# Kernel optimization log

Hardware: AMD Instinct MI355X
Metric: run time of the kernel (lower is better)

Reference implementation:

```python
import jax, jax.numpy as jnp
import numpy as np
import math

B, C, N = 8, 512, 2048

def setup_inputs() -> dict:
    key = jax.random.key(0)
    ks = jax.random.split(key, 7)
    s = 0.02
    return {
        "x": jax.random.normal(ks[0], (B, C, N), dtype=jnp.float32),
        "Wq": jax.random.normal(ks[1], (C // 2, C), dtype=jnp.float32) * s,
        "bq": jax.random.normal(ks[2], (C // 2,), dtype=jnp.float32) * s,
        "Wk": jax.random.normal(ks[3], (C // 2, C), dtype=jnp.float32) * s,
        "bk": jax.random.normal(ks[4], (C // 2,), dtype=jnp.float32) * s,
        "Wv": jax.random.normal(ks[5], (C, C), dtype=jnp.float32) * s,
        "bv": jax.random.normal(ks[6], (C,), dtype=jnp.float32) * s,
    }

def reference(x, Wq, bq, Wk, bk, Wv, bv):
    # pointwise conv1d == channel matmul: (O,C) x (B,C,N) -> (B,O,N)
    Q = jnp.einsum('oc,bcn->bon', Wq, x) + bq[None, :, None]  # (B, C/2, N)
    K = jnp.einsum('oc,bcn->bon', Wk, x) + bk[None, :, None]  # (B, C/2, N)
    V = jnp.einsum('oc,bcn->bon', Wv, x) + bv[None, :, None]  # (B, C, N)
    scale = 1.0 / math.sqrt(K.shape[1])
    A = jnp.einsum('bcn,bcm->bnm', Q, K) * scale              # (B, N, N)
    A = jax.nn.softmax(A, axis=-1)
    out = jnp.einsum('bcm,bnm->bcn', V, A)                    # V @ A^T
    return x + out
```

## Files before the change

### kernel.cpp

```cpp
#include <hip/hip_runtime.h>

#define B_ 8
#define C_ 512
#define N_ 2048
#define O_ 256

typedef unsigned short u16;
typedef unsigned char u8;
typedef unsigned int uint;
typedef __bf16 bf16x8 __attribute__((ext_vector_type(8)));
typedef float f32x4 __attribute__((ext_vector_type(4)));
typedef int i32x8 __attribute__((ext_vector_type(8)));

#define AS1 __attribute__((address_space(1)))
#define AS3 __attribute__((address_space(3)))

__device__ __forceinline__ u16 f2bf(float f) {
  union { float f; unsigned u; } v; v.f = f;
  return (u16)((v.u + 0x7fffu + ((v.u >> 16) & 1u)) >> 16);
}

__device__ __forceinline__ uint pk4_e4m3(float a, float b, float c, float d) {
  int r = __builtin_amdgcn_cvt_pk_fp8_f32(a, b, 0, false);
  r = __builtin_amdgcn_cvt_pk_fp8_f32(c, d, r, true);
  return (uint)r;
}

__device__ __forceinline__ void mfma_mainloop(
    const u16* __restrict__ Ag, int lda,
    const u16* __restrict__ Bg, int ldb, int K,
    u16 (&As)[128][64], u16 (&Bs)[128][64], f32x4 (&acc)[4][4])
{
  const int t = threadIdx.x;
  const int lane = t & 63;
  const int w = t >> 6;
  const int wm = (w >> 1) * 64, wn = (w & 1) * 64;
  const int lrow = lane & 15, quad = lane >> 4;
  const int r8 = lane >> 3;
  const int kgsrc = (lane & 7) ^ r8;
  const int swz = lrow & 7;

  for (int k0 = 0; k0 < K; k0 += 64) {
#pragma unroll
    for (int i = 0; i < 4; i++) {
      int row = w * 32 + i * 8;
      __builtin_amdgcn_global_load_lds(
          (const AS1 uint*)(Ag + (size_t)(row + r8) * lda + k0 + kgsrc * 8),
          (AS3 uint*)(&As[row][0]), 16, 0, 0);
      __builtin_amdgcn_global_load_lds(
          (const AS1 uint*)(Bg + (size_t)(row + r8) * ldb + k0 + kgsrc * 8),
          (AS3 uint*)(&Bs[row][0]), 16, 0, 0);
    }
    __syncthreads();
#pragma unroll
    for (int kk = 0; kk < 2; kk++) {
      const int pg = (kk * 4 + quad) ^ swz;
      bf16x8 af[4], bfr[4];
#pragma unroll
      for (int i = 0; i < 4; i++)
        af[i] = *(const bf16x8*)(&As[wm + i * 16 + lrow][pg * 8]);
#pragma unroll
      for (int j = 0; j < 4; j++)
        bfr[j] = *(const bf16x8*)(&Bs[wn + j * 16 + lrow][pg * 8]);
#pragma unroll
      for (int i = 0; i < 4; i++)
#pragma unroll
        for (int j = 0; j < 4; j++)
          acc[i][j] = __builtin_amdgcn_mfma_f32_16x16x32_bf16(af[i], bfr[j], acc[i][j], 0, 0, 0);
    }
    __syncthreads();
  }
}

union MxFrag { i32x8 v; uint4 q[2]; };

__device__ __forceinline__ void mx_mainloop(
    const u8* __restrict__ Ag, int lda,
    const u8* __restrict__ Bg, int ldb, int K,
    u8 (&As)[128][128], u8 (&Bs)[128][128], f32x4 (&acc)[4][4])
{
  const int t = threadIdx.x;
  const int lane = t & 63;
  const int w = t >> 6;
  const int wm = (w >> 1) * 64, wn = (w & 1) * 64;
  const int lrow = lane & 15, quad = lane >> 4;
  const int swz = lrow & 7;
  const int r8 = lane >> 3;
  const int gsrc = (lane & 7) ^ r8;

  for (int k0 = 0; k0 < K; k0 += 128) {
#pragma unroll
    for (int i = 0; i < 4; i++) {
      int row = i * 32 + w * 8;
      __builtin_amdgcn_global_load_lds(
          (const AS1 uint*)(Ag + (size_t)(row + r8) * lda + k0 + gsrc * 16),
          (AS3 uint*)(&As[row][0]), 16, 0, 0);
      __builtin_amdgcn_global_load_lds(
          (const AS1 uint*)(Bg + (size_t)(row + r8) * ldb + k0 + gsrc * 16),
          (AS3 uint*)(&Bs[row][0]), 16, 0, 0);
    }
    __syncthreads();
    const int g0 = (quad * 2) ^ swz, g1 = (quad * 2 + 1) ^ swz;
    MxFrag af[4], bfr[4];
#pragma unroll
    for (int i = 0; i < 4; i++) {
      const u8* rp = &As[wm + i * 16 + lrow][0];
      af[i].q[0] = *(const uint4*)(rp + g0 * 16);
      af[i].q[1] = *(const uint4*)(rp + g1 * 16);
    }
#pragma unroll
    for (int j = 0; j < 4; j++) {
      const u8* rp = &Bs[wn + j * 16 + lrow][0];
      bfr[j].q[0] = *(const uint4*)(rp + g0 * 16);
      bfr[j].q[1] = *(const uint4*)(rp + g1 * 16);
    }
#pragma unroll
    for (int i = 0; i < 4; i++)
#pragma unroll
      for (int j = 0; j < 4; j++)
        acc[i][j] = __builtin_amdgcn_mfma_scale_f32_16x16x128_f8f6f4(
            af[i].v, bfr[j].v, acc[i][j],
            0, 0,
            0, 0x7f7f7f7f,
            0, 0x7f7f7f7f);
    __syncthreads();
  }
}

__global__ __launch_bounds__(256) void convert_w_kernel(
    const float* __restrict__ Wq, const float* __restrict__ Wk,
    const float* __restrict__ Wv,
    u16* __restrict__ Wqb, u16* __restrict__ Wkb, u16* __restrict__ Wvb,
    float* __restrict__ rowsum)
{
  int i = blockIdx.x * 256 + threadIdx.x;
  if (i < O_ * C_) { Wqb[i] = f2bf(Wq[i]); Wkb[i] = f2bf(Wk[i]); }
  Wvb[i] = f2bf(Wv[i]);
  if (i < B_ * N_) rowsum[i] = 0.f;
}

__global__ __launch_bounds__(256) void transpose_kernel(
    const float* __restrict__ x, u16* __restrict__ xT)
{
  __shared__ u16 tile[64][72];
  int b = blockIdx.z;
  int n0 = blockIdx.x * 64, c0 = blockIdx.y * 64;
  int t = threadIdx.x;
  const float* src = x + (size_t)b * C_ * N_ + (size_t)c0 * N_ + n0;
  int r = t >> 4;
  int f4 = (t & 15) * 4;
#pragma unroll
  for (int i = 0; i < 4; i++) {
    int c = r + 16 * i;
    float4 v = *(const float4*)(src + (size_t)c * N_ + f4);
    tile[f4 + 0][c] = f2bf(v.x);
    tile[f4 + 1][c] = f2bf(v.y);
    tile[f4 + 2][c] = f2bf(v.z);
    tile[f4 + 3][c] = f2bf(v.w);
  }
  __syncthreads();
  u16* dst = xT + (size_t)b * N_ * C_ + (size_t)n0 * C_ + c0;
  int nr = t >> 3;
  int cc = (t & 7) * 8;
#pragma unroll
  for (int i = 0; i < 2; i++) {
    int n = nr + 32 * i;
    *(uint4*)(dst + (size_t)n * C_ + cc) = *(const uint4*)(&tile[n][cc]);
  }
}

__global__ __launch_bounds__(256) void proj_all_kernel(
    const u16* __restrict__ xT,
    const u16* __restrict__ Wqb, const float* __restrict__ bq,
    const u16* __restrict__ Wkb, const float* __restrict__ bk,
    const u16* __restrict__ Wvb, const float* __restrict__ bv,
    u8* __restrict__ Qt8, u8* __restrict__ Kt8, u8* __restrict__ V8)
{
  __shared__ u16 As[128][64], Bs[128][64];
  const int n0 = blockIdx.x * 128;
  const int b = blockIdx.y;
  const int sub = blockIdx.z;
  const u16* xTb = xT + (size_t)b * N_ * C_ + (size_t)n0 * C_;

  const f32x4 zero = {0.f, 0.f, 0.f, 0.f};
  f32x4 acc[4][4];
#pragma unroll
  for (int i = 0; i < 4; i++)
#pragma unroll
    for (int j = 0; j < 4; j++) acc[i][j] = zero;

  const int lane = threadIdx.x & 63;
  const int w = threadIdx.x >> 6;
  const int wm = (w >> 1) * 64, wn = (w & 1) * 64;
  const int quad = lane >> 4, lcol = lane & 15;

  if (sub < 4) {
    const int isK = sub >> 1;
    const int o0 = (sub & 1) * 128;
    const u16* Wg = (isK ? Wkb : Wqb) + (size_t)o0 * C_;
    const float* bias = isK ? bk : bq;
    u8* outp = (isK ? Kt8 : Qt8) + (size_t)b * N_ * O_;

    mfma_mainloop(Wg, C_, xTb, C_, C_, As, Bs, acc);

#pragma unroll
    for (int i = 0; i < 4; i++) {
      int obase = o0 + wm + i * 16 + quad * 4;
      float4 bb = *(const float4*)(bias + obase);
#pragma unroll
      for (int j = 0; j < 4; j++) {
        int n = n0 + wn + j * 16 + lcol;
        uint d = pk4_e4m3(acc[i][j][0] + bb.x, acc[i][j][1] + bb.y,
                          acc[i][j][2] + bb.z, acc[i][j][3] + bb.w);
        *(uint*)(outp + (size_t)n * O_ + obase) = d;
      }
    }
  } else {
    const int c0 = (sub - 4) * 128;
    const u16* Wg = Wvb + (size_t)c0 * C_;
    u8* outp = V8 + (size_t)b * C_ * N_;

    mfma_mainloop(xTb, C_, Wg, C_, C_, As, Bs, acc);

#pragma unroll
    for (int j = 0; j < 4; j++) {
      int c = c0 + wn + j * 16 + lcol;
      float bb = bv[c];
#pragma unroll
      for (int i = 0; i < 4; i++) {
        int nbase = n0 + wm + i * 16 + quad * 4;
        uint d = pk4_e4m3(acc[i][j][0] + bb, acc[i][j][1] + bb,
                          acc[i][j][2] + bb, acc[i][j][3] + bb);
        *(uint*)(outp + (size_t)c * N_ + nbase) = d;
      }
    }
  }
}

__global__ __launch_bounds__(256) void attn_s_kernel(
    const u8* __restrict__ Qt8, const u8* __restrict__ Kt8,
    u8* __restrict__ P, float* __restrict__ rowsum)
{
  __shared__ __align__(16) u8 As[128][128], Bs[128][128];
  int b = blockIdx.z;
  int m0 = blockIdx.x * 128, n0 = blockIdx.y * 128;
  const u8* Ag = Kt8 + (size_t)b * N_ * O_ + (size_t)m0 * O_;
  const u8* Bg = Qt8 + (size_t)b * N_ * O_ + (size_t)n0 * O_;

  const f32x4 zero = {0.f, 0.f, 0.f, 0.f};
  f32x4 acc[4][4];
#pragma unroll
  for (int i = 0; i < 4; i++)
#pragma unroll
    for (int j = 0; j < 4; j++) acc[i][j] = zero;

  mx_mainloop(Ag, O_, Bg, O_, O_, As, Bs, acc);

  u8* Pp = P + (size_t)b * N_ * N_;
  float* rs = rowsum + (size_t)b * N_;
  const int lane = threadIdx.x & 63;
  const int w = threadIdx.x >> 6;
  const int wm = (w >> 1) * 64, wn = (w & 1) * 64;
  const int quad = lane >> 4, lcol = lane & 15;

  float partial[4];
#pragma unroll
  for (int j = 0; j < 4; j++) partial[j] = 0.f;

#pragma unroll
  for (int j = 0; j < 4; j++) {
    int n = n0 + wn + j * 16 + lcol;
#pragma unroll
    for (int i = 0; i < 4; i++) {
      int mbase = m0 + wm + i * 16 + quad * 4;
      float p0 = __expf(acc[i][j][0] * 0.0625f);
      float p1 = __expf(acc[i][j][1] * 0.0625f);
      float p2 = __expf(acc[i][j][2] * 0.0625f);
      float p3 = __expf(acc[i][j][3] * 0.0625f);
      *(uint*)(Pp + (size_t)n * N_ + mbase) = pk4_e4m3(p0, p1, p2, p3);
      partial[j] += p0 + p1 + p2 + p3;
    }
  }
#pragma unroll
  for (int msk = 16; msk < 64; msk <<= 1)
#pragma unroll
    for (int j = 0; j < 4; j++)
      partial[j] += __shfl_xor(partial[j], msk);
  if (quad == 0) {
#pragma unroll
    for (int j = 0; j < 4; j++)
      atomicAdd(&rs[n0 + wn + j * 16 + lcol], partial[j]);
  }
}

__global__ __launch_bounds__(256) void attn_o_kernel(
    const u8* __restrict__ V, const u8* __restrict__ P,
    const float* __restrict__ rowsum, const float* __restrict__ x,
    float* __restrict__ out)
{
  __shared__ __align__(16) u8 As[128][128], Bs[128][128];
  int b = blockIdx.z;
  int c0 = blockIdx.y * 128, n0 = blockIdx.x * 128;
  const u8* Ag = V + (size_t)b * C_ * N_ + (size_t)c0 * N_;
  const u8* Bg = P + (size_t)b * N_ * N_ + (size_t)n0 * N_;

  const f32x4 zero = {0.f, 0.f, 0.f, 0.f};
  f32x4 acc[4][4];
#pragma unroll
  for (int i = 0; i < 4; i++)
#pragma unroll
    for (int j = 0; j < 4; j++) acc[i][j] = zero;

  mx_mainloop(Ag, N_, Bg, N_, N_, As, Bs, acc);

  const int lane = threadIdx.x & 63;
  const int w = threadIdx.x >> 6;
  const int wm = (w >> 1) * 64, wn = (w & 1) * 64;
  const int quad = lane >> 4, lrow = lane & 15;

  const float* xb = x + (size_t)b * C_ * N_;
  float* ob = out + (size_t)b * C_ * N_;
  float invl[4];
#pragma unroll
  for (int j = 0; j < 4; j++)
    invl[j] = 1.f / rowsum[b * N_ + n0 + wn + j * 16 + lrow];

#pragma unroll
  for (int i = 0; i < 4; i++)
#pragma unroll
    for (int rr = 0; rr < 4; rr++) {
      int c = c0 + wm + i * 16 + quad * 4 + rr;
#pragma unroll
      for (int j = 0; j < 4; j++) {
        int n = n0 + wn + j * 16 + lrow;
        size_t idx = (size_t)c * N_ + n;
        ob[idx] = xb[idx] + acc[i][j][rr] * invl[j];
      }
    }
}

extern "C" void kernel_launch(void* const* d_in, const int* in_sizes, int n_in,
                              void* d_out, int out_size, void* d_ws, size_t ws_size,
                              hipStream_t stream)
{
  (void)in_sizes; (void)n_in; (void)out_size; (void)ws_size;
  const float* x  = (const float*)d_in[0];
  const float* Wq = (const float*)d_in[1];
  const float* bq = (const float*)d_in[2];
  const float* Wk = (const float*)d_in[3];
  const float* bk = (const float*)d_in[4];
  const float* Wv = (const float*)d_in[5];
  const float* bv = (const float*)d_in[6];
  float* out = (float*)d_out;

  char* ws = (char*)d_ws;
  size_t off = 0;
  auto carve = [&](size_t bytes) -> char* {
    char* p = ws + off;
    off += (bytes + 255) & ~(size_t)255;
    return p;
  };
  u16* xT   = (u16*)carve((size_t)B_ * N_ * C_ * 2);
  u16* Wqb  = (u16*)carve((size_t)O_ * C_ * 2);
  u16* Wkb  = (u16*)carve((size_t)O_ * C_ * 2);
  u16* Wvb  = (u16*)carve((size_t)C_ * C_ * 2);
  u8*  Qt8  = (u8*) carve((size_t)B_ * N_ * O_);
  u8*  Kt8  = (u8*) carve((size_t)B_ * N_ * O_);
  u8*  Vb   = (u8*) carve((size_t)B_ * C_ * N_);
  u8*  P    = (u8*) carve((size_t)B_ * N_ * N_);
  float* rowsum = (float*)carve((size_t)B_ * N_ * 4);

  convert_w_kernel<<<dim3((C_ * C_) / 256), 256, 0, stream>>>(
      Wq, Wk, Wv, Wqb, Wkb, Wvb, rowsum);
  transpose_kernel<<<dim3(N_ / 64, C_ / 64, B_), 256, 0, stream>>>(x, xT);
  proj_all_kernel<<<dim3(N_ / 128, B_, 8), 256, 0, stream>>>(
      xT, Wqb, bq, Wkb, bk, Wvb, bv, Qt8, Kt8, Vb);
  attn_s_kernel<<<dim3(N_ / 128, N_ / 128, B_), 256, 0, stream>>>(Qt8, Kt8, P, rowsum);
  attn_o_kernel<<<dim3(N_ / 128, C_ / 128, B_), 256, 0, stream>>>(Vb, P, rowsum, x, out);
}
```

Before: 179.8 us.

## Switch projections to FP8 MX MFMA, fuse prep kernels, halve attn_o tile

Casts x and the weights to FP8 e4m3, where they were bf16 before, and runs the Q/K/V projections with the scaled f8f6f4 MFMA mainloop in place of the bf16 one. The weight conversion and the transpose of x are merged into one prep kernel, removing a launch and halving the bytes written for xT. The attn_o kernel moves to a 64x128 tile with twice the blocks, for more parallelism and occupancy. Quantising the inputs to FP8 before the projections lowers accuracy and may push the output closer to the tolerance limit.

```diff
diff --git a/kernel.cpp b/kernel.cpp
--- a/kernel.cpp
+++ b/kernel.cpp
@@ -8,7 +8,6 @@
 typedef unsigned short u16;
 typedef unsigned char u8;
 typedef unsigned int uint;
-typedef __bf16 bf16x8 __attribute__((ext_vector_type(8)));
 typedef float f32x4 __attribute__((ext_vector_type(4)));
 typedef int i32x8 __attribute__((ext_vector_type(8)));
 
@@ -19,57 +18,13 @@
   union { float f; unsigned u; } v; v.f = f;
   return (u16)((v.u + 0x7fffu + ((v.u >> 16) & 1u)) >> 16);
 }
-
+__device__ __forceinline__ float bf2f(u16 h) {
+  union { uint u; float f; } v; v.u = ((uint)h) << 16; return v.f;
+}
 __device__ __forceinline__ uint pk4_e4m3(float a, float b, float c, float d) {
   int r = __builtin_amdgcn_cvt_pk_fp8_f32(a, b, 0, false);
   r = __builtin_amdgcn_cvt_pk_fp8_f32(c, d, r, true);
   return (uint)r;
-}
-
-__device__ __forceinline__ void mfma_mainloop(
-    const u16* __restrict__ Ag, int lda,
-    const u16* __restrict__ Bg, int ldb, int K,
-    u16 (&As)[128][64], u16 (&Bs)[128][64], f32x4 (&acc)[4][4])
-{
-  const int t = threadIdx.x;
-  const int lane = t & 63;
-  const int w = t >> 6;
-  const int wm = (w >> 1) * 64, wn = (w & 1) * 64;
-  const int lrow = lane & 15, quad = lane >> 4;
-  const int r8 = lane >> 3;
-  const int kgsrc = (lane & 7) ^ r8;
-  const int swz = lrow & 7;
-
-  for (int k0 = 0; k0 < K; k0 += 64) {
-#pragma unroll
-    for (int i = 0; i < 4; i++) {
-      int row = w * 32 + i * 8;
-      __builtin_amdgcn_global_load_lds(
-          (const AS1 uint*)(Ag + (size_t)(row + r8) * lda + k0 + kgsrc * 8),
-          (AS3 uint*)(&As[row][0]), 16, 0, 0);
-      __builtin_amdgcn_global_load_lds(
-          (const AS1 uint*)(Bg + (size_t)(row + r8) * ldb + k0 + kgsrc * 8),
-          (AS3 uint*)(&Bs[row][0]), 16, 0, 0);
-    }
-    __syncthreads();
-#pragma unroll
-    for (int kk = 0; kk < 2; kk++) {
-      const int pg = (kk * 4 + quad) ^ swz;
-      bf16x8 af[4], bfr[4];
-#pragma unroll
-      for (int i = 0; i < 4; i++)
-        af[i] = *(const bf16x8*)(&As[wm + i * 16 + lrow][pg * 8]);
-#pragma unroll
-      for (int j = 0; j < 4; j++)
-        bfr[j] = *(const bf16x8*)(&Bs[wn + j * 16 + lrow][pg * 8]);
-#pragma unroll
-      for (int i = 0; i < 4; i++)
-#pragma unroll
-        for (int j = 0; j < 4; j++)
-          acc[i][j] = __builtin_amdgcn_mfma_f32_16x16x32_bf16(af[i], bfr[j], acc[i][j], 0, 0, 0);
-    }
-    __syncthreads();
-  }
 }
 
 union MxFrag { i32x8 v; uint4 q[2]; };
@@ -127,60 +82,73 @@
   }
 }
 
-__global__ __launch_bounds__(256) void convert_w_kernel(
+__global__ __launch_bounds__(256) void prep_kernel(
+    const float* __restrict__ x,
     const float* __restrict__ Wq, const float* __restrict__ Wk,
     const float* __restrict__ Wv,
-    u16* __restrict__ Wqb, u16* __restrict__ Wkb, u16* __restrict__ Wvb,
-    float* __restrict__ rowsum)
-{
-  int i = blockIdx.x * 256 + threadIdx.x;
-  if (i < O_ * C_) { Wqb[i] = f2bf(Wq[i]); Wkb[i] = f2bf(Wk[i]); }
-  Wvb[i] = f2bf(Wv[i]);
-  if (i < B_ * N_) rowsum[i] = 0.f;
-}
-
-__global__ __launch_bounds__(256) void transpose_kernel(
-    const float* __restrict__ x, u16* __restrict__ xT)
+    u8* __restrict__ xT8, u8* __restrict__ Wq8, u8* __restrict__ Wk8,
+    u8* __restrict__ Wv8, float* __restrict__ rowsum)
 {
   __shared__ u16 tile[64][72];
-  int b = blockIdx.z;
-  int n0 = blockIdx.x * 64, c0 = blockIdx.y * 64;
-  int t = threadIdx.x;
-  const float* src = x + (size_t)b * C_ * N_ + (size_t)c0 * N_ + n0;
-  int r = t >> 4;
-  int f4 = (t & 15) * 4;
-#pragma unroll
-  for (int i = 0; i < 4; i++) {
-    int c = r + 16 * i;
-    float4 v = *(const float4*)(src + (size_t)c * N_ + f4);
-    tile[f4 + 0][c] = f2bf(v.x);
-    tile[f4 + 1][c] = f2bf(v.y);
-    tile[f4 + 2][c] = f2bf(v.z);
-    tile[f4 + 3][c] = f2bf(v.w);
-  }
-  __syncthreads();
-  u16* dst = xT + (size_t)b * N_ * C_ + (size_t)n0 * C_ + c0;
-  int nr = t >> 3;
-  int cc = (t & 7) * 8;
-#pragma unroll
-  for (int i = 0; i < 2; i++) {
-    int n = nr + 32 * i;
-    *(uint4*)(dst + (size_t)n * C_ + cc) = *(const uint4*)(&tile[n][cc]);
+  const int bid = blockIdx.x;
+  const int t = threadIdx.x;
+  if (bid < 2048) {
+    int b = bid >> 8;
+    int n0 = (bid & 31) * 64;
+    int c0 = ((bid >> 5) & 7) * 64;
+    const float* src = x + (size_t)b * C_ * N_ + (size_t)c0 * N_ + n0;
+    int r = t >> 4;
+    int f4 = (t & 15) * 4;
+#pragma unroll
+    for (int i = 0; i < 4; i++) {
+      int c = r + 16 * i;
+      float4 v = *(const float4*)(src + (size_t)c * N_ + f4);
+      tile[f4 + 0][c] = f2bf(v.x);
+      tile[f4 + 1][c] = f2bf(v.y);
+      tile[f4 + 2][c] = f2bf(v.z);
+      tile[f4 + 3][c] = f2bf(v.w);
+    }
+    __syncthreads();
+    u8* dst = xT8 + (size_t)b * N_ * C_ + (size_t)n0 * C_ + c0;
+    int n = t >> 2;
+    int cc = (t & 3) * 16;
+    uint4 d;
+    d.x = pk4_e4m3(bf2f(tile[n][cc + 0]), bf2f(tile[n][cc + 1]),
+                   bf2f(tile[n][cc + 2]), bf2f(tile[n][cc + 3]));
+    d.y = pk4_e4m3(bf2f(tile[n][cc + 4]), bf2f(tile[n][cc + 5]),
+                   bf2f(tile[n][cc + 6]), bf2f(tile[n][cc + 7]));
+    d.z = pk4_e4m3(bf2f(tile[n][cc + 8]), bf2f(tile[n][cc + 9]),
+                   bf2f(tile[n][cc + 10]), bf2f(tile[n][cc + 11]));
+    d.w = pk4_e4m3(bf2f(tile[n][cc + 12]), bf2f(tile[n][cc + 13]),
+                   bf2f(tile[n][cc + 14]), bf2f(tile[n][cc + 15]));
+    *(uint4*)(dst + (size_t)n * C_ + cc) = d;
+  } else {
+    int gid = (bid - 2048) * 256 + t;
+    const float* src; u8* dst; int o;
+    if (gid < 32768)      { src = Wq; dst = Wq8; o = gid; }
+    else if (gid < 65536) { src = Wk; dst = Wk8; o = gid - 32768; }
+    else                  { src = Wv; dst = Wv8; o = gid - 65536; }
+    float4 v = *(const float4*)(src + (size_t)o * 4);
+    *(uint*)(dst + (size_t)o * 4) = pk4_e4m3(v.x, v.y, v.z, v.w);
+    if (gid < 4096) {
+      float4 z = {0.f, 0.f, 0.f, 0.f};
+      *(float4*)(rowsum + gid * 4) = z;
+    }
   }
 }
 
 __global__ __launch_bounds__(256) void proj_all_kernel(
-    const u16* __restrict__ xT,
-    const u16* __restrict__ Wqb, const float* __restrict__ bq,
-    const u16* __restrict__ Wkb, const float* __restrict__ bk,
-    const u16* __restrict__ Wvb, const float* __restrict__ bv,
+    const u8* __restrict__ xT8,
+    const u8* __restrict__ Wq8, const float* __restrict__ bq,
+    const u8* __restrict__ Wk8, const float* __restrict__ bk,
+    const u8* __restrict__ Wv8, const float* __restrict__ bv,
     u8* __restrict__ Qt8, u8* __restrict__ Kt8, u8* __restrict__ V8)
 {
-  __shared__ u16 As[128][64], Bs[128][64];
+  __shared__ __align__(16) u8 As[128][128], Bs[128][128];
   const int n0 = blockIdx.x * 128;
   const int b = blockIdx.y;
   const int sub = blockIdx.z;
-  const u16* xTb = xT + (size_t)b * N_ * C_ + (size_t)n0 * C_;
+  const u8* xTb = xT8 + (size_t)b * N_ * C_ + (size_t)n0 * C_;
 
   const f32x4 zero = {0.f, 0.f, 0.f, 0.f};
   f32x4 acc[4][4];
@@ -197,11 +165,11 @@
   if (sub < 4) {
     const int isK = sub >> 1;
     const int o0 = (sub & 1) * 128;
-    const u16* Wg = (isK ? Wkb : Wqb) + (size_t)o0 * C_;
+    const u8* Wg = (isK ? Wk8 : Wq8) + (size_t)o0 * C_;
     const float* bias = isK ? bk : bq;
     u8* outp = (isK ? Kt8 : Qt8) + (size_t)b * N_ * O_;
 
-    mfma_mainloop(Wg, C_, xTb, C_, C_, As, Bs, acc);
+    mx_mainloop(Wg, C_, xTb, C_, C_, As, Bs, acc);
 
 #pragma unroll
     for (int i = 0; i < 4; i++) {
@@ -217,10 +185,10 @@
     }
   } else {
     const int c0 = (sub - 4) * 128;
-    const u16* Wg = Wvb + (size_t)c0 * C_;
+    const u8* Wg = Wv8 + (size_t)c0 * C_;
     u8* outp = V8 + (size_t)b * C_ * N_;
 
-    mfma_mainloop(xTb, C_, Wg, C_, C_, As, Bs, acc);
+    mx_mainloop(xTb, C_, Wg, C_, C_, As, Bs, acc);
 
 #pragma unroll
     for (int j = 0; j < 4; j++) {
@@ -298,25 +266,68 @@
     const float* __restrict__ rowsum, const float* __restrict__ x,
     float* __restrict__ out)
 {
-  __shared__ __align__(16) u8 As[128][128], Bs[128][128];
-  int b = blockIdx.z;
-  int c0 = blockIdx.y * 128, n0 = blockIdx.x * 128;
+  __shared__ __align__(16) u8 As[64][128], Bs[128][128];
+  const int b = blockIdx.z;
+  const int c0 = blockIdx.y * 64, n0 = blockIdx.x * 128;
   const u8* Ag = V + (size_t)b * C_ * N_ + (size_t)c0 * N_;
   const u8* Bg = P + (size_t)b * N_ * N_ + (size_t)n0 * N_;
 
+  const int t = threadIdx.x;
+  const int lane = t & 63;
+  const int w = t >> 6;
+  const int wm = (w >> 1) * 32;
+  const int wn = (w & 1) * 64;
+  const int lrow = lane & 15, quad = lane >> 4;
+  const int swz = lrow & 7;
+  const int r8 = lane >> 3;
+  const int gsrc = (lane & 7) ^ r8;
+
   const f32x4 zero = {0.f, 0.f, 0.f, 0.f};
-  f32x4 acc[4][4];
-#pragma unroll
-  for (int i = 0; i < 4; i++)
+  f32x4 acc[2][4];
+#pragma unroll
+  for (int i = 0; i < 2; i++)
 #pragma unroll
     for (int j = 0; j < 4; j++) acc[i][j] = zero;
 
-  mx_mainloop(Ag, N_, Bg, N_, N_, As, Bs, acc);
-
-  const int lane = threadIdx.x & 63;
-  const int w = threadIdx.x >> 6;
-  const int wm = (w >> 1) * 64, wn = (w & 1) * 64;
-  const int quad = lane >> 4, lrow = lane & 15;
+  for (int k0 = 0; k0 < N_; k0 += 128) {
+#pragma unroll
+    for (int s = 0; s < 2; s++) {
+      int row = (w * 2 + s) * 8;
+      __builtin_amdgcn_global_load_lds(
+          (const AS1 uint*)(Ag + (size_t)(row + r8) * N_ + k0 + gsrc * 16),
+          (AS3 uint*)(&As[row][0]), 16, 0, 0);
+    }
+#pragma unroll
+    for (int s = 0; s < 4; s++) {
+      int row = (w * 4 + s) * 8;
+      __builtin_amdgcn_global_load_lds(
+          (const AS1 uint*)(Bg + (size_t)(row + r8) * N_ + k0 + gsrc * 16),
+          (AS3 uint*)(&Bs[row][0]), 16, 0, 0);
+    }
+    __syncthreads();
+    const int g0 = (quad * 2) ^ swz, g1 = (quad * 2 + 1) ^ swz;
+    MxFrag af[2], bfr[4];
+#pragma unroll
+    for (int i = 0; i < 2; i++) {
+      const u8* rp = &As[wm + i * 16 + lrow][0];
+      af[i].q[0] = *(const uint4*)(rp + g0 * 16);
+      af[i].q[1] = *(const uint4*)(rp + g1 * 16);
+    }
+#pragma unroll
+    for (int j = 0; j < 4; j++) {
+      const u8* rp = &Bs[wn + j * 16 + lrow][0];
+      bfr[j].q[0] = *(const uint4*)(rp + g0 * 16);
+      bfr[j].q[1] = *(const uint4*)(rp + g1 * 16);
+    }
+#pragma unroll
+    for (int i = 0; i < 2; i++)
+#pragma unroll
+      for (int j = 0; j < 4; j++)
+        acc[i][j] = __builtin_amdgcn_mfma_scale_f32_16x16x128_f8f6f4(
+            af[i].v, bfr[j].v, acc[i][j],
+            0, 0, 0, 0x7f7f7f7f, 0, 0x7f7f7f7f);
+    __syncthreads();
+  }
 
   const float* xb = x + (size_t)b * C_ * N_;
   float* ob = out + (size_t)b * C_ * N_;
@@ -326,7 +337,7 @@
     invl[j] = 1.f / rowsum[b * N_ + n0 + wn + j * 16 + lrow];
 
 #pragma unroll
-  for (int i = 0; i < 4; i++)
+  for (int i = 0; i < 2; i++)
 #pragma unroll
     for (int rr = 0; rr < 4; rr++) {
       int c = c0 + wm + i * 16 + quad * 4 + rr;
@@ -360,21 +371,20 @@
     off += (bytes + 255) & ~(size_t)255;
     return p;
   };
-  u16* xT   = (u16*)carve((size_t)B_ * N_ * C_ * 2);
-  u16* Wqb  = (u16*)carve((size_t)O_ * C_ * 2);
-  u16* Wkb  = (u16*)carve((size_t)O_ * C_ * 2);
-  u16* Wvb  = (u16*)carve((size_t)C_ * C_ * 2);
+  u8*  xT8  = (u8*) carve((size_t)B_ * N_ * C_);
+  u8*  Wq8  = (u8*) carve((size_t)O_ * C_);
+  u8*  Wk8  = (u8*) carve((size_t)O_ * C_);
+  u8*  Wv8  = (u8*) carve((size_t)C_ * C_);
   u8*  Qt8  = (u8*) carve((size_t)B_ * N_ * O_);
   u8*  Kt8  = (u8*) carve((size_t)B_ * N_ * O_);
   u8*  Vb   = (u8*) carve((size_t)B_ * C_ * N_);
   u8*  P    = (u8*) carve((size_t)B_ * N_ * N_);
   float* rowsum = (float*)carve((size_t)B_ * N_ * 4);
 
-  convert_w_kernel<<<dim3((C_ * C_) / 256), 256, 0, stream>>>(
-      Wq, Wk, Wv, Wqb, Wkb, Wvb, rowsum);
-  transpose_kernel<<<dim3(N_ / 64, C_ / 64, B_), 256, 0, stream>>>(x, xT);
+  prep_kernel<<<dim3(2560), 256, 0, stream>>>(
+      x, Wq, Wk, Wv, xT8, Wq8, Wk8, Wv8, rowsum);
   proj_all_kernel<<<dim3(N_ / 128, B_, 8), 256, 0, stream>>>(
-      xT, Wqb, bq, Wkb, bk, Wvb, bv, Qt8, Kt8, Vb);
+      xT8, Wq8, bq, Wk8, bk, Wv8, bv, Qt8, Kt8, Vb);
   attn_s_kernel<<<dim3(N_ / 128, N_ / 128, B_), 256, 0, stream>>>(Qt8, Kt8, P, rowsum);
-  attn_o_kernel<<<dim3(N_ / 128, C_ / 128, B_), 256, 0, stream>>>(Vb, P, rowsum, x, out);
-}
+  attn_o_kernel<<<dim3(N_ / 128, C_ / 64, B_), 256, 0, stream>>>(Vb, P, rowsum, x, out);
+}
```

Measured after the change: 167.3 us. 1.07x faster.
